# Optimization experiments

Hardware: AMD Instinct MI355X
Metric: run time of the kernel (lower is better)

Reference implementation:

```python
import jax, jax.numpy as jnp
import numpy as np

FP8_E4M3_MAX = 448.0  # max finite value of float8_e4m3fn
SCALE = 2.0          # input activation scale
WEIGHT_SCALE = 2.0   # weight scale
IN_FEATURES = 4096
OUT_FEATURES = 4096
M = 4096


def setup_inputs() -> dict:
    key = jax.random.key(0)
    k_in, k_w, k_b = jax.random.split(key, 3)
    inp = jax.random.normal(k_in, (M, IN_FEATURES), dtype=jnp.float32)
    # weight is stored in fp8 e4m3fn in the module; materialize the fp8-quantized
    # values (cast randn -> fp8 -> back) so float32 array holds exact fp8 grid values
    w_raw = jax.random.normal(k_w, (OUT_FEATURES, IN_FEATURES), dtype=jnp.float32)
    weight = w_raw.astype(jnp.float8_e4m3fn).astype(jnp.float32)
    bias = jax.random.normal(k_b, (OUT_FEATURES,), dtype=jnp.float32)
    return {"input": inp, "weight": weight, "bias": bias}


def _quant_dequant_fp8(x, scale):
    # quantize_affine_float8: clamp(x/scale) to fp8 range, cast to e4m3fn;
    # dequantize: cast back to float and multiply by scale
    q = jnp.clip(x / scale, -FP8_E4M3_MAX, FP8_E4M3_MAX).astype(jnp.float8_e4m3fn)
    return q.astype(jnp.float32) * scale


def reference(input, weight, bias):
    # dequantize fp8 weight (values already on fp8 grid): w_fp32 = w * weight_scale
    w_dq = weight * WEIGHT_SCALE                     # [out, in]
    dq_input = _quant_dequant_fp8(input, SCALE)      # [M, in]
    out = jnp.einsum("mi,oi->mo", dq_input, w_dq)    # fp32 GEMM
    return out + bias
```

## Files before the change

### kernel.cpp

```cpp
#include <hip/hip_runtime.h>
#include <hip/hip_bf16.h>
#include <stdint.h>


typedef __attribute__((ext_vector_type(4))) float f32x4;
typedef __attribute__((ext_vector_type(2))) int i32x2;
typedef __attribute__((ext_vector_type(4))) int i32x4;
typedef __attribute__((ext_vector_type(8))) int i32x8;

#define FP8_MAX 448.0f
#define UNIT_SCALE 0x7F7F7F7F

__global__ void quant_fp8_kernel(const float* __restrict__ x,
                                 uint32_t* __restrict__ q,
                                 float mul, int n8) {
    int i = blockIdx.x * blockDim.x + threadIdx.x;
    if (i >= n8) return;
    const float4* xv = (const float4*)x;
    float4 v0 = xv[2 * i];
    float4 v1 = xv[2 * i + 1];
    float a[8] = {v0.x, v0.y, v0.z, v0.w, v1.x, v1.y, v1.z, v1.w};
#pragma unroll
    for (int j = 0; j < 8; ++j) {
        float t = a[j] * mul;
        t = fminf(fmaxf(t, -FP8_MAX), FP8_MAX);
        a[j] = t;
    }
    int lo = 0, hi = 0;
    lo = __builtin_amdgcn_cvt_pk_fp8_f32(a[0], a[1], lo, false);
    lo = __builtin_amdgcn_cvt_pk_fp8_f32(a[2], a[3], lo, true);
    hi = __builtin_amdgcn_cvt_pk_fp8_f32(a[4], a[5], hi, false);
    hi = __builtin_amdgcn_cvt_pk_fp8_f32(a[6], a[7], hi, true);
    i32x2 out;
    out.x = lo;
    out.y = hi;
    ((i32x2*)q)[i] = out;
}

#define KTILES 32

__device__ static inline void gload_lds16(const void* g, void* l) {
    __builtin_amdgcn_global_load_lds(
        (const __attribute__((address_space(1))) void*)g,
        (__attribute__((address_space(3))) void*)l, 16, 0, 0);
}

#define STAGE2(GSRC, KB, LBASE, C0)                                        \
    gload_lds16((GSRC) + (KB) + (C0) * 32,       (LBASE) + (C0) * 8192 + t * 16); \
    gload_lds16((GSRC) + (KB) + (C0) * 32 + 32,  (LBASE) + (C0) * 8192 + 8192 + t * 16);

#define READ_A(LBASE, MH)                                                  \
    _Pragma("unroll") for (int m = 0; m < 4; ++m) {                        \
        i32x4 lo = *(const i32x4*)((LBASE) + aoff + (MH) * 1024 + m * 256);       \
        i32x4 hi = *(const i32x4*)((LBASE) + aoff + (MH) * 1024 + m * 256 + 4096);\
        areg[m] = (i32x8){lo[0], lo[1], lo[2], lo[3], hi[0], hi[1], hi[2], hi[3]};\
    }

#define READ_B(LBASE, NH)                                                  \
    _Pragma("unroll") for (int n = 0; n < 2; ++n) {                        \
        i32x4 lo = *(const i32x4*)((LBASE) + boff + (NH) * 512 + n * 256);        \
        i32x4 hi = *(const i32x4*)((LBASE) + boff + (NH) * 512 + n * 256 + 4096); \
        breg[n] = (i32x8){lo[0], lo[1], lo[2], lo[3], hi[0], hi[1], hi[2], hi[3]};\
    }

#define MFMA8(MH, NH)                                                      \
    __builtin_amdgcn_s_setprio(1);                                         \
    _Pragma("unroll") for (int m = 0; m < 4; ++m)                          \
        _Pragma("unroll") for (int n = 0; n < 2; ++n)                      \
            acc[(MH) * 4 + m][(NH) * 2 + n] =                              \
                __builtin_amdgcn_mfma_scale_f32_16x16x128_f8f6f4(          \
                    areg[m], breg[n], acc[(MH) * 4 + m][(NH) * 2 + n],     \
                    0, 0, 0, UNIT_SCALE, 0, UNIT_SCALE);                   \
    __builtin_amdgcn_s_setprio(0);

#define BAR() __builtin_amdgcn_s_barrier()
#define VMW2() asm volatile("s_waitcnt vmcnt(2)" ::: "memory")

__global__ __launch_bounds__(512, 2) void fp8_gemm_bias_kernel(
        const uint8_t* __restrict__ Aq, const uint8_t* __restrict__ Wq,
        const float* __restrict__ bias, float* __restrict__ C,
        int M, int N, int K) {
    __shared__ __align__(16) uint8_t lds[131072];
    uint8_t* const sA0 = lds;
    uint8_t* const sB0 = lds + 32768;
    uint8_t* const sA1 = lds + 65536;
    uint8_t* const sB1 = lds + 98304;

    const int t = threadIdx.x;
    const int lane = t & 63;
    const int w = t >> 6;
    const int wr = w >> 2;
    const int wc = w & 3;
    const int lr = lane & 15;
    const int lk = lane >> 4;

    const int bid = blockIdx.x;
    const int swz = (bid & 7) * 32 + (bid >> 3);
    const int bm = swz >> 4;
    const int bn = swz & 15;

    const uint8_t* Abase = Aq + (size_t)(bm * 256) * K;
    const uint8_t* Bbase = Wq + (size_t)(bn * 256) * K;

    const int srow = t & 255;
    const int scol = (t >> 8) * 16;
    const uint8_t* gA = Abase + (size_t)srow * K + scol;
    const uint8_t* gB = Bbase + (size_t)srow * K + scol;

    const int aoff = lk * 8192 + wr * 2048 + lr * 16;
    const int boff = lk * 8192 + wc * 1024 + lr * 16;

    f32x4 acc[8][4];
#pragma unroll
    for (int mi = 0; mi < 8; ++mi)
#pragma unroll
        for (int ni = 0; ni < 4; ++ni)
            acc[mi][ni] = (f32x4){0.f, 0.f, 0.f, 0.f};

    i32x8 areg[4], breg[2];

    STAGE2(gA, 0, sA0, 0)
    STAGE2(gA, 0, sA0, 2)
    STAGE2(gB, 0, sB0, 0)
    STAGE2(gB, 0, sB0, 2)
    STAGE2(gA, 128, sA1, 0)
    VMW2();
    BAR();

    for (int it = 0; it < KTILES / 2; ++it) {
        const int kb1 = (2 * it + 1) * 128;
        const int kb2 = ((2 * it + 2) & 31) * 128;
        const int kb3 = ((2 * it + 3) & 31) * 128;

        READ_A(sA0, 0)
        READ_B(sB0, 0)
        STAGE2(gA, kb1, sA1, 2)
        BAR();
        MFMA8(0, 0)
        BAR();
        READ_B(sB0, 1)
        STAGE2(gB, kb1, sB1, 0)
        BAR();
        MFMA8(0, 1)
        BAR();
        READ_A(sA0, 1)
        READ_B(sB0, 0)
        STAGE2(gB, kb1, sB1, 2)
        BAR();
        MFMA8(1, 0)
        BAR();
        READ_B(sB0, 1)
        STAGE2(gA, kb2, sA0, 0)
        BAR();
        MFMA8(1, 1)
        VMW2();
        BAR();

        READ_A(sA1, 0)
        READ_B(sB1, 0)
        STAGE2(gA, kb2, sA0, 2)
        BAR();
        MFMA8(0, 0)
        BAR();
        READ_B(sB1, 1)
        STAGE2(gB, kb2, sB0, 0)
        BAR();
        MFMA8(0, 1)
        BAR();
        READ_A(sA1, 1)
        READ_B(sB1, 0)
        STAGE2(gB, kb2, sB0, 2)
        BAR();
        MFMA8(1, 0)
        BAR();
        READ_B(sB1, 1)
        STAGE2(gA, kb3, sA1, 0)
        BAR();
        MFMA8(1, 1)
        VMW2();
        BAR();
    }

    const int crow0 = bm * 256 + wr * 128 + lk * 4;
    const int ccol0 = bn * 256 + wc * 64 + lr;
#pragma unroll
    for (int ni = 0; ni < 4; ++ni) {
        const int col = ccol0 + ni * 16;
        const float bv = bias[col];
#pragma unroll
        for (int mi = 0; mi < 8; ++mi) {
            const int row = crow0 + mi * 16;
#pragma unroll
            for (int j = 0; j < 4; ++j) {
                C[(size_t)(row + j) * N + col] = acc[mi][ni][j] * 4.0f + bv;
            }
        }
    }
}

extern "C" void kernel_launch(void* const* d_in, const int* in_sizes, int n_in,
                              void* d_out, int out_size, void* d_ws, size_t ws_size,
                              hipStream_t stream) {
    const int M = 4096, N = 4096, K = 4096;
    const float* input  = (const float*)d_in[0];
    const float* weight = (const float*)d_in[1];
    const float* bias   = (const float*)d_in[2];
    float* out = (float*)d_out;

    uint8_t* Aq = (uint8_t*)d_ws;
    uint8_t* Wq = (uint8_t*)d_ws + (size_t)M * K;

    {
        int n8 = (M * K) / 8;
        int blocks = (n8 + 255) / 256;
        quant_fp8_kernel<<<blocks, 256, 0, stream>>>(input, (uint32_t*)Aq, 0.5f, n8);
        quant_fp8_kernel<<<blocks, 256, 0, stream>>>(weight, (uint32_t*)Wq, 1.0f, n8);
    }

    dim3 grid(256);
    fp8_gemm_bias_kernel<<<grid, 512, 0, stream>>>(Aq, Wq, bias, out, M, N, K);
}
```

Before: 124.8 us.

## Coarsen GEMM pipeline to full-tile stages with 16-MFMA phases

Restructures the main loop from four 8-MFMA phases per k-tile with half-tile async loads into two 16-MFMA phases per k-tile. All four B fragments are now read once per tile, and each A or B tile is loaded in full in a single stage. This cuts barriers and redundant B LDS reads in half. In exchange, prefetch lookahead shrinks, since each half-iteration now ends with a vmcnt(0) wait instead of vmcnt(2). B register usage also doubles, which adds pressure at two waves per SIMD.

```diff
diff --git a/kernel.cpp b/kernel.cpp
--- a/kernel.cpp
+++ b/kernel.cpp
@@ -45,9 +45,11 @@
         (__attribute__((address_space(3))) void*)l, 16, 0, 0);
 }
 
-#define STAGE2(GSRC, KB, LBASE, C0)                                        \
-    gload_lds16((GSRC) + (KB) + (C0) * 32,       (LBASE) + (C0) * 8192 + t * 16); \
-    gload_lds16((GSRC) + (KB) + (C0) * 32 + 32,  (LBASE) + (C0) * 8192 + 8192 + t * 16);
+#define STAGE_FULL(GSRC, KB, LBASE)                                        \
+    gload_lds16((GSRC) + (KB),       (LBASE) + t * 16);                    \
+    gload_lds16((GSRC) + (KB) + 32,  (LBASE) + 8192  + t * 16);            \
+    gload_lds16((GSRC) + (KB) + 64,  (LBASE) + 16384 + t * 16);            \
+    gload_lds16((GSRC) + (KB) + 96,  (LBASE) + 24576 + t * 16);
 
 #define READ_A(LBASE, MH)                                                  \
     _Pragma("unroll") for (int m = 0; m < 4; ++m) {                        \
@@ -56,25 +58,25 @@
         areg[m] = (i32x8){lo[0], lo[1], lo[2], lo[3], hi[0], hi[1], hi[2], hi[3]};\
     }
 
-#define READ_B(LBASE, NH)                                                  \
-    _Pragma("unroll") for (int n = 0; n < 2; ++n) {                        \
-        i32x4 lo = *(const i32x4*)((LBASE) + boff + (NH) * 512 + n * 256);        \
-        i32x4 hi = *(const i32x4*)((LBASE) + boff + (NH) * 512 + n * 256 + 4096); \
+#define READ_B_ALL(LBASE)                                                  \
+    _Pragma("unroll") for (int n = 0; n < 4; ++n) {                        \
+        i32x4 lo = *(const i32x4*)((LBASE) + boff + n * 256);                     \
+        i32x4 hi = *(const i32x4*)((LBASE) + boff + n * 256 + 4096);              \
         breg[n] = (i32x8){lo[0], lo[1], lo[2], lo[3], hi[0], hi[1], hi[2], hi[3]};\
     }
 
-#define MFMA8(MH, NH)                                                      \
+#define MFMA16(MH)                                                         \
     __builtin_amdgcn_s_setprio(1);                                         \
     _Pragma("unroll") for (int m = 0; m < 4; ++m)                          \
-        _Pragma("unroll") for (int n = 0; n < 2; ++n)                      \
-            acc[(MH) * 4 + m][(NH) * 2 + n] =                              \
+        _Pragma("unroll") for (int n = 0; n < 4; ++n)                      \
+            acc[(MH) * 4 + m][n] =                                         \
                 __builtin_amdgcn_mfma_scale_f32_16x16x128_f8f6f4(          \
-                    areg[m], breg[n], acc[(MH) * 4 + m][(NH) * 2 + n],     \
+                    areg[m], breg[n], acc[(MH) * 4 + m][n],                \
                     0, 0, 0, UNIT_SCALE, 0, UNIT_SCALE);                   \
     __builtin_amdgcn_s_setprio(0);
 
 #define BAR() __builtin_amdgcn_s_barrier()
-#define VMW2() asm volatile("s_waitcnt vmcnt(2)" ::: "memory")
+#define VM0() asm volatile("s_waitcnt vmcnt(0)" ::: "memory")
 
 __global__ __launch_bounds__(512, 2) void fp8_gemm_bias_kernel(
         const uint8_t* __restrict__ Aq, const uint8_t* __restrict__ Wq,
@@ -117,67 +119,41 @@
         for (int ni = 0; ni < 4; ++ni)
             acc[mi][ni] = (f32x4){0.f, 0.f, 0.f, 0.f};
 
-    i32x8 areg[4], breg[2];
+    i32x8 areg[4], breg[4];
 
-    STAGE2(gA, 0, sA0, 0)
-    STAGE2(gA, 0, sA0, 2)
-    STAGE2(gB, 0, sB0, 0)
-    STAGE2(gB, 0, sB0, 2)
-    STAGE2(gA, 128, sA1, 0)
-    VMW2();
+    STAGE_FULL(gA, 0, sA0)
+    STAGE_FULL(gB, 0, sB0)
+    VM0();
     BAR();
 
     for (int it = 0; it < KTILES / 2; ++it) {
         const int kb1 = (2 * it + 1) * 128;
         const int kb2 = ((2 * it + 2) & 31) * 128;
-        const int kb3 = ((2 * it + 3) & 31) * 128;
 
         READ_A(sA0, 0)
-        READ_B(sB0, 0)
-        STAGE2(gA, kb1, sA1, 2)
+        READ_B_ALL(sB0)
+        STAGE_FULL(gA, kb1, sA1)
         BAR();
-        MFMA8(0, 0)
-        BAR();
-        READ_B(sB0, 1)
-        STAGE2(gB, kb1, sB1, 0)
-        BAR();
-        MFMA8(0, 1)
+        MFMA16(0)
         BAR();
         READ_A(sA0, 1)
-        READ_B(sB0, 0)
-        STAGE2(gB, kb1, sB1, 2)
+        STAGE_FULL(gB, kb1, sB1)
         BAR();
-        MFMA8(1, 0)
-        BAR();
-        READ_B(sB0, 1)
-        STAGE2(gA, kb2, sA0, 0)
-        BAR();
-        MFMA8(1, 1)
-        VMW2();
+        MFMA16(1)
+        VM0();
         BAR();
 
         READ_A(sA1, 0)
-        READ_B(sB1, 0)
-        STAGE2(gA, kb2, sA0, 2)
+        READ_B_ALL(sB1)
+        STAGE_FULL(gA, kb2, sA0)
         BAR();
-        MFMA8(0, 0)
-        BAR();
-        READ_B(sB1, 1)
-        STAGE2(gB, kb2, sB0, 0)
-        BAR();
-        MFMA8(0, 1)
+        MFMA16(0)
         BAR();
         READ_A(sA1, 1)
-        READ_B(sB1, 0)
-        STAGE2(gB, kb2, sB0, 2)
+        STAGE_FULL(gB, kb2, sB0)
         BAR();
-        MFMA8(1, 0)
-        BAR();
-        READ_B(sB1, 1)
-        STAGE2(gA, kb3, sA1, 0)
-        BAR();
-        MFMA8(1, 1)
-        VMW2();
+        MFMA16(1)
+        VM0();
         BAR();
     }
 
```

Result: slower. 135.6 us (+8.7%).
